# Performance work log

Measured on AMD Instinct MI355X. Metric: run time of the kernel, lower is better.

The kernel has to match this reference:

```python
import jax, jax.numpy as jnp
import numpy as np

B, CIN, H, W = 256, 1280, 7, 7
A, NCLS, HID, NGT = 9, 20, 128, 40
OUT_DIM = 5 * A + NCLS  # 65


def setup_inputs() -> dict:
    key = jax.random.key(0)
    ks = jax.random.split(key, 8)
    features = jax.random.normal(ks[0], (B, CIN, H, W), jnp.float32)
    # grid: (x, y) centers of each feature cell, in feature-map coordinates
    grid = jax.random.uniform(ks[1], (B, H, W, 2), jnp.float32) * 7.0
    # GT boxes (x1, y1, x2, y2, class), padded count NGT per image
    xy1 = jax.random.uniform(ks[2], (B, NGT, 2), jnp.float32) * 5.0
    wh = jax.random.uniform(ks[3], (B, NGT, 2), jnp.float32) * 2.0 + 0.5
    cls = jax.random.randint(ks[4], (B, NGT, 1), 0, NCLS).astype(jnp.float32)
    bboxes = jnp.concatenate([xy1, xy1 + wh, cls], axis=-1)
    # anchor shapes (w, h) as in SingleStageDetector.__init__
    anc = jnp.array([[1.0, 1], [2, 2], [3, 3], [4, 4], [5, 5],
                     [2, 3], [3, 2], [3, 5], [5, 3]], jnp.float32)
    W1 = jax.random.normal(ks[5], (HID, CIN), jnp.float32) * 0.02
    b1 = jnp.zeros((HID,), jnp.float32)
    W2 = jax.random.normal(ks[6], (OUT_DIM, HID), jnp.float32) * 0.02
    b2 = jnp.zeros((OUT_DIM,), jnp.float32)
    return dict(features=features, grid=grid, bboxes=bboxes, anc=anc,
                W1=W1, b1=b1, W2=W2, b2=b2)


def reference(features, grid, bboxes, anc, W1, b1, W2, b2):
    Bx = features.shape[0]
    # --- PredictionNetwork (inference mode; dropout is identity at eval) ---
    h = jnp.einsum('bchw,oc->bohw', features, W1) + b1[None, :, None, None]
    h = jax.nn.leaky_relu(h, negative_slope=0.01)
    out = jnp.einsum('bchw,oc->bohw', h, W2) + b2[None, :, None, None]
    conf_scores = jax.nn.sigmoid(out[:, 4 * A:5 * A])          # (B, A, H, W)
    offsets = out[:, :4 * A].reshape(Bx, A, 4, H, W)
    offsets = jnp.concatenate(
        [jax.nn.sigmoid(offsets[:, :, :2]) - 0.5, offsets[:, :, 2:]], axis=2)
    class_scores = out[:, 5 * A:]                               # (B, C, H, W)
    # --- GenerateAnchor: (B, A, H, W, 4) as (x_tl, y_tl, x_br, y_br) ---
    ctr = grid[:, None]                    # (B, 1, H, W, 2)
    half = anc[None, :, None, None, :] / 2  # (1, A, 1, 1, 2)
    anchors = jnp.concatenate([ctr - half, ctr + half], axis=-1)
    # --- IoU: (B, A*H*W, N) ---
    P = anchors.reshape(Bx, -1, 4)          # (B, AHW, 4)
    gt = bboxes[..., :4]                    # (B, N, 4)
    tl = jnp.maximum(P[:, :, None, :2], gt[:, None, :, :2])
    br = jnp.minimum(P[:, :, None, 2:], gt[:, None, :, 2:])
    inter = jnp.prod(jnp.clip(br - tl, 0.0), axis=-1)  # (B, AHW, N)
    # torch code zeroes intersections for proposals with any coord <= 0
    legal = (jnp.min(P, axis=-1) > 0)[..., None]
    inter = inter * legal
    p_area = ((P[:, :, 2] - P[:, :, 0]) * (P[:, :, 3] - P[:, :, 1]))[:, :, None]
    g_area = ((gt[:, :, 2] - gt[:, :, 0]) * (gt[:, :, 3] - gt[:, :, 1]))[:, None, :]
    iou_mat = inter / (g_area + p_area - inter)
    return (conf_scores, offsets, class_scores, iou_mat)
```

## Files before the change

kernel.cpp:

```cpp
#include <hip/hip_runtime.h>


#define CIN_  1280
#define HW_   49
#define HID_  128
#define OUTD_ 65
#define NGT_  40
#define NP_   441

#define CONF_OFF 0
#define OFFS_OFF 112896
#define CLS_OFF  564480
#define IOU_OFF  815360

#define WS_W1F_U32 81920u
#define WS_W2F_U32 5120u

typedef __bf16 bf16x8 __attribute__((ext_vector_type(8)));
typedef float  f32x4  __attribute__((ext_vector_type(4)));

__device__ __forceinline__ unsigned pack2bf(float lo, float hi) {
    unsigned a = __float_as_uint(lo);
    unsigned b = __float_as_uint(hi);
    a = (a + 0x7FFFu + ((a >> 16) & 1u)) >> 16;
    b = (b + 0x7FFFu + ((b >> 16) & 1u)) >> 16;
    return a | (b << 16);
}
__device__ __forceinline__ float sigmoidf_(float v) { return 1.f / (1.f + __expf(-v)); }

__device__ __forceinline__ bf16x8 ld_frag(const unsigned* p) {
    union { uint4 u; bf16x8 v; } x;
    x.u = *(const uint4*)p;
    return x.v;
}
__device__ __forceinline__ bf16x8 as_bf(uint4 u) {
    union { uint4 u; bf16x8 v; } x; x.u = u; return x.v;
}

__global__ __launch_bounds__(256) void prep_w(
    const float* __restrict__ W1, const float* __restrict__ W2,
    unsigned* __restrict__ ws)
{
    int X = blockIdx.x * 256 + threadIdx.x;
    if (X < (int)WS_W1F_U32) {
        int sub = X & 3, lane = (X >> 2) & 63, f = X >> 8;
        int mt = f & 7, K32 = f >> 3;
        int o = mt * 16 + (lane & 15);
        int c = K32 * 32 + (lane >> 4) * 8 + sub * 2;
        float2 v = *(const float2*)(W1 + o * CIN_ + c);
        ws[X] = pack2bf(v.x, v.y);
    } else {
        int Y = X - (int)WS_W1F_U32;
        int sub = Y & 3, lane = (Y >> 2) & 63, f = Y >> 8;
        int mt2 = f % 5, ks2 = f / 5;
        int o2 = mt2 * 16 + (lane & 15);
        int c = ks2 * 32 + (lane >> 4) * 8 + sub * 2;
        unsigned val = 0;
        if (o2 < OUTD_) {
            float2 v = *(const float2*)(W2 + o2 * HID_ + c);
            val = pack2bf(v.x, v.y);
        }
        ws[WS_W1F_U32 + Y] = val;
    }
}

__global__ __launch_bounds__(512, 8) void fused_main(
    const float* __restrict__ F,
    const float* __restrict__ grd,
    const float* __restrict__ bbox,
    const float* __restrict__ anc,
    const unsigned* __restrict__ wsW,
    const float* __restrict__ B1,
    const float* __restrict__ B2,
    float* __restrict__ out)
{
    __shared__ __align__(16) unsigned lds[16 * 640];
    unsigned* smHT = lds;

    const int tid  = threadIdx.x;
    const int b    = blockIdx.x >> 2;
    const int qtr  = blockIdx.x & 3;
    const int lane = tid & 63;
    const int w    = tid >> 6;
    const int quad = lane >> 4;
    const int m16  = lane & 15;
    const int hw0  = qtr * 16;

    const float* Fb = F + b * (CIN_ * HW_);

    #pragma unroll
    for (int g = 0; g < 4; ++g) {
        float f0[5], f1[5];
        #pragma unroll
        for (int u = 0; u < 5; ++u) {
            int i   = (g * 5 + u) * 512 + tid;
            int cp  = i >> 4;
            int row = i & 15;
            int hw  = hw0 + row;
            bool ok = hw < HW_;
            f0[u] = ok ? Fb[(2 * cp) * HW_ + hw] : 0.f;
            f1[u] = ok ? Fb[(2 * cp + 1) * HW_ + hw] : 0.f;
        }
        #pragma unroll
        for (int u = 0; u < 5; ++u) {
            int i   = (g * 5 + u) * 512 + tid;
            int cp  = i >> 4;
            int row = i & 15;
            int cb = cp >> 2, sub = cp & 3;
            lds[row * 640 + ((cb ^ (row & 7)) << 2) + sub] = pack2bf(f0[u], f1[u]);
        }
    }
    __syncthreads();

    const uint4* Ap = (const uint4*)wsW + w * 64 + lane;
    const unsigned* r0b = lds + m16 * 640;
    const int swz = (m16 & 7);

    f32x4 acc0 = (f32x4)(0.f);
    uint4 a0 = Ap[0];
    uint4 a1 = Ap[512];
    for (int k = 0; k < 40; ++k) {
        uint4 an;
        if (k < 38) an = Ap[(k + 2) * 512];
        int off = ((k * 4 + quad) ^ swz) << 2;
        acc0 = __builtin_amdgcn_mfma_f32_16x16x32_bf16(as_bf(a0), ld_frag(r0b + off), acc0, 0, 0, 0);
        a0 = a1; a1 = an;
    }

    uint4 a20 = {}, a21 = {}, a22 = {}, a23 = {};
    if (w < 5) {
        const uint4* A2p = (const uint4*)(wsW + WS_W1F_U32) + w * 64 + lane;
        a20 = A2p[0]; a21 = A2p[320]; a22 = A2p[640]; a23 = A2p[960];
    }

    __syncthreads();

    #pragma unroll
    for (int rp = 0; rp < 2; ++rp) {
        int o0 = w * 16 + quad * 4 + 2 * rp;
        float v0 = acc0[2 * rp]     + B1[o0];
        float v1 = acc0[2 * rp + 1] + B1[o0 + 1];
        v0 = v0 > 0.f ? v0 : 0.01f * v0;
        v1 = v1 > 0.f ? v1 : 0.01f * v1;
        smHT[m16 * 68 + (o0 >> 1)] = pack2bf(v0, v1);
    }
    __syncthreads();

    if (w < 5) {
        f32x4 c2 = (f32x4)(0.f);
        const unsigned* Bb = smHT + m16 * 68 + quad * 4;
        c2 = __builtin_amdgcn_mfma_f32_16x16x32_bf16(as_bf(a20), ld_frag(Bb +  0), c2, 0, 0, 0);
        c2 = __builtin_amdgcn_mfma_f32_16x16x32_bf16(as_bf(a21), ld_frag(Bb + 16), c2, 0, 0, 0);
        c2 = __builtin_amdgcn_mfma_f32_16x16x32_bf16(as_bf(a22), ld_frag(Bb + 32), c2, 0, 0, 0);
        c2 = __builtin_amdgcn_mfma_f32_16x16x32_bf16(as_bf(a23), ld_frag(Bb + 48), c2, 0, 0, 0);
        int hw = hw0 + m16;
        if (hw < HW_) {
            #pragma unroll
            for (int r = 0; r < 4; ++r) {
                int o2 = w * 16 + quad * 4 + r;
                if (o2 >= OUTD_) continue;
                float aa = c2[r] + B2[o2];
                unsigned dst; float val;
                if (o2 < 36) {
                    int an9 = o2 >> 2, kk = o2 & 3;
                    val = (kk < 2) ? (sigmoidf_(aa) - 0.5f) : aa;
                    dst = OFFS_OFF + b * 1764 + an9 * 196 + kk * 49 + hw;
                } else if (o2 < 45) {
                    val = sigmoidf_(aa);
                    dst = CONF_OFF + b * 441 + (o2 - 36) * 49 + hw;
                } else {
                    val = aa;
                    dst = CLS_OFF + b * 980 + (o2 - 45) * 49 + hw;
                }
                out[dst] = val;
            }
        }
    }

    {
        int gl = (lane < NGT_) ? lane : 0;
        const float* gb = bbox + b * 200 + gl * 5;
        float gx1 = gb[0], gy1 = gb[1], gx2 = gb[2], gy2 = gb[3];
        float gA = (gx2 - gx1) * (gy2 - gy1);
        const int pstart = (qtr * NP_) >> 2;
        const int pend   = ((qtr + 1) * NP_) >> 2;
        #pragma unroll 4
        for (int p = pstart + w; p < pend; p += 8) {
            int a9 = p / 49, r = p - a9 * 49;
            float2 ct = *(const float2*)(grd + b * 98 + 2 * r);
            float hx = anc[2 * a9] * 0.5f,  hy = anc[2 * a9 + 1] * 0.5f;
            float px1 = ct.x - hx, py1 = ct.y - hy, px2 = ct.x + hx, py2 = ct.y + hy;
            float pA = (px2 - px1) * (py2 - py1);
            float legal = (fminf(fminf(px1, py1), fminf(px2, py2)) > 0.f) ? 1.f : 0.f;
            float tlx = fmaxf(px1, gx1), tly = fmaxf(py1, gy1);
            float brx = fminf(px2, gx2), bry = fminf(py2, gy2);
            float dx = fmaxf(brx - tlx, 0.f), dy = fmaxf(bry - tly, 0.f);
            float inter = dx * dy * legal;
            float iou = inter / (gA + pA - inter);
            if (lane < NGT_)
                out[IOU_OFF + b * (NP_ * NGT_) + p * 40 + lane] = iou;
        }
    }
}

extern "C" void kernel_launch(void* const* d_in, const int* in_sizes, int n_in,
                              void* d_out, int out_size, void* d_ws, size_t ws_size,
                              hipStream_t stream) {
    const float* F  = (const float*)d_in[0];
    const float* G  = (const float*)d_in[1];
    const float* BB = (const float*)d_in[2];
    const float* AN = (const float*)d_in[3];
    const float* W1 = (const float*)d_in[4];
    const float* B1 = (const float*)d_in[5];
    const float* W2 = (const float*)d_in[6];
    const float* B2 = (const float*)d_in[7];
    float* out = (float*)d_out;
    unsigned* wsu = (unsigned*)d_ws;

    prep_w<<<340, 256, 0, stream>>>(W1, W2, wsu);
    fused_main<<<1024, 512, 0, stream>>>(F, G, BB, AN, wsu, B1, B2, out);
}
```

Before: 145.6 us.

## Process one image per block with double-buffered async feature staging into LDS

Instead of four blocks per image each gathering a strided 16-pixel slice, each block now handles a whole image. It streams contiguous 256-channel fp32 feature chunks into LDS with global_load_lds, double-buffered across five chunks. Features are converted to bf16 fragments when read from LDS, and each wave computes a 2x2 tile of MFMA outputs, so W1 fragments are fetched once per image instead of four times. The goal is to replace uncoalesced strided global reads and repeated weight traffic with coalesced async copies that overlap compute. The cost is only 256 blocks of 8 waves with about 100KB of LDS each, and padded rows that read neighbouring channel data which is then discarded. Smaller tweaks switch bf16 packing to a native conversion and IoU division to __fdividef.

```diff
diff --git a/kernel.cpp b/kernel.cpp
--- a/kernel.cpp
+++ b/kernel.cpp
@@ -16,15 +16,15 @@
 #define WS_W1F_U32 81920u
 #define WS_W2F_U32 5120u
 
+#define CHUNK_DW 12544
+
 typedef __bf16 bf16x8 __attribute__((ext_vector_type(8)));
 typedef float  f32x4  __attribute__((ext_vector_type(4)));
 
 __device__ __forceinline__ unsigned pack2bf(float lo, float hi) {
-    unsigned a = __float_as_uint(lo);
-    unsigned b = __float_as_uint(hi);
-    a = (a + 0x7FFFu + ((a >> 16) & 1u)) >> 16;
-    b = (b + 0x7FFFu + ((b >> 16) & 1u)) >> 16;
-    return a | (b << 16);
+    unsigned short a = __builtin_bit_cast(unsigned short, (__bf16)lo);
+    unsigned short b = __builtin_bit_cast(unsigned short, (__bf16)hi);
+    return (unsigned)a | ((unsigned)b << 16);
 }
 __device__ __forceinline__ float sigmoidf_(float v) { return 1.f / (1.f + __expf(-v)); }
 
@@ -35,6 +35,18 @@
 }
 __device__ __forceinline__ bf16x8 as_bf(uint4 u) {
     union { uint4 u; bf16x8 v; } x; x.u = u; return x.v;
+}
+__device__ __forceinline__ bf16x8 frag_from_f32(const float* p) {
+    union { unsigned u[4]; bf16x8 v; } x;
+    #pragma unroll
+    for (int j = 0; j < 4; ++j)
+        x.u[j] = pack2bf(p[(2 * j) * 49], p[(2 * j + 1) * 49]);
+    return x.v;
+}
+__device__ __forceinline__ void gload_lds16(const float* g, unsigned* l) {
+    __builtin_amdgcn_global_load_lds(
+        (const __attribute__((address_space(1))) unsigned*)g,
+        (__attribute__((address_space(3))) unsigned*)l, 16, 0, 0);
 }
 
 __global__ __launch_bounds__(256) void prep_w(
@@ -64,7 +76,7 @@
     }
 }
 
-__global__ __launch_bounds__(512, 8) void fused_main(
+__global__ __launch_bounds__(512, 2) void fused_main(
     const float* __restrict__ F,
     const float* __restrict__ grd,
     const float* __restrict__ bbox,
@@ -74,90 +86,102 @@
     const float* __restrict__ B2,
     float* __restrict__ out)
 {
-    __shared__ __align__(16) unsigned lds[16 * 640];
+    __shared__ __align__(16) unsigned lds[2 * CHUNK_DW + 64];
     unsigned* smHT = lds;
 
     const int tid  = threadIdx.x;
-    const int b    = blockIdx.x >> 2;
-    const int qtr  = blockIdx.x & 3;
+    const int b    = blockIdx.x;
     const int lane = tid & 63;
     const int w    = tid >> 6;
+    const int wo   = w >> 1;
+    const int wh   = w & 1;
     const int quad = lane >> 4;
     const int m16  = lane & 15;
-    const int hw0  = qtr * 16;
 
     const float* Fb = F + b * (CIN_ * HW_);
 
+    #define STAGE(c)                                                         \
+        {                                                                    \
+            const float* srcb = Fb + (c) * CHUNK_DW;                         \
+            unsigned*    dstb = lds + (((c) & 1) ? CHUNK_DW : 0);            \
+            _Pragma("unroll")                                                \
+            for (int i = 0; i < 6; ++i) {                                    \
+                int s0 = w * 1536 + i * 256;                                 \
+                gload_lds16(srcb + s0 + lane * 4, dstb + s0);                \
+            }                                                                \
+            if (w == 7) gload_lds16(srcb + 12288 + lane * 4, dstb + 12288);  \
+        }
+
+    STAGE(0);
+    __syncthreads();
+
+    const uint4* Af = (const uint4*)wsW;
+    f32x4 acc[2][2] = {{(f32x4)(0.f), (f32x4)(0.f)}, {(f32x4)(0.f), (f32x4)(0.f)}};
+
     #pragma unroll
-    for (int g = 0; g < 4; ++g) {
-        float f0[5], f1[5];
+    for (int c = 0; c < 5; ++c) {
+        uint4 Ar[8][2];
         #pragma unroll
-        for (int u = 0; u < 5; ++u) {
-            int i   = (g * 5 + u) * 512 + tid;
-            int cp  = i >> 4;
-            int row = i & 15;
-            int hw  = hw0 + row;
-            bool ok = hw < HW_;
-            f0[u] = ok ? Fb[(2 * cp) * HW_ + hw] : 0.f;
-            f1[u] = ok ? Fb[(2 * cp + 1) * HW_ + hw] : 0.f;
-        }
+        for (int kk = 0; kk < 8; ++kk) {
+            #pragma unroll
+            for (int mo = 0; mo < 2; ++mo)
+                Ar[kk][mo] = Af[(((c * 8 + kk) * 8) + (wo * 2 + mo)) * 64 + lane];
+        }
+        __builtin_amdgcn_sched_barrier(0);
+        if (c < 4) STAGE(c + 1);
+        __builtin_amdgcn_sched_barrier(0);
+
+        const float* fb = (const float*)(lds + ((c & 1) ? CHUNK_DW : 0));
         #pragma unroll
-        for (int u = 0; u < 5; ++u) {
-            int i   = (g * 5 + u) * 512 + tid;
-            int cp  = i >> 4;
-            int row = i & 15;
-            int cb = cp >> 2, sub = cp & 3;
-            lds[row * 640 + ((cb ^ (row & 7)) << 2) + sub] = pack2bf(f0[u], f1[u]);
+        for (int kk = 0; kk < 8; ++kk) {
+            bf16x8 A0 = as_bf(Ar[kk][0]);
+            bf16x8 A1 = as_bf(Ar[kk][1]);
+            #pragma unroll
+            for (int nh = 0; nh < 2; ++nh) {
+                const float* pb = fb + (kk * 32 + quad * 8) * 49
+                                     + (wh * 32 + nh * 16 + m16);
+                bf16x8 Bf = frag_from_f32(pb);
+                acc[0][nh] = __builtin_amdgcn_mfma_f32_16x16x32_bf16(A0, Bf, acc[0][nh], 0, 0, 0);
+                acc[1][nh] = __builtin_amdgcn_mfma_f32_16x16x32_bf16(A1, Bf, acc[1][nh], 0, 0, 0);
+            }
+        }
+        __builtin_amdgcn_sched_barrier(0);
+        __syncthreads();
+    }
+
+    #pragma unroll
+    for (int mo = 0; mo < 2; ++mo) {
+        #pragma unroll
+        for (int nh = 0; nh < 2; ++nh) {
+            int row = (wh * 2 + nh) * 16 + m16;
+            #pragma unroll
+            for (int rp = 0; rp < 2; ++rp) {
+                int o0 = (wo * 2 + mo) * 16 + quad * 4 + 2 * rp;
+                float v0 = acc[mo][nh][2 * rp]     + B1[o0];
+                float v1 = acc[mo][nh][2 * rp + 1] + B1[o0 + 1];
+                v0 = v0 > 0.f ? v0 : 0.01f * v0;
+                v1 = v1 > 0.f ? v1 : 0.01f * v1;
+                smHT[row * 68 + (o0 >> 1)] = pack2bf(v0, v1);
+            }
         }
     }
     __syncthreads();
 
-    const uint4* Ap = (const uint4*)wsW + w * 64 + lane;
-    const unsigned* r0b = lds + m16 * 640;
-    const int swz = (m16 & 7);
-
-    f32x4 acc0 = (f32x4)(0.f);
-    uint4 a0 = Ap[0];
-    uint4 a1 = Ap[512];
-    for (int k = 0; k < 40; ++k) {
-        uint4 an;
-        if (k < 38) an = Ap[(k + 2) * 512];
-        int off = ((k * 4 + quad) ^ swz) << 2;
-        acc0 = __builtin_amdgcn_mfma_f32_16x16x32_bf16(as_bf(a0), ld_frag(r0b + off), acc0, 0, 0, 0);
-        a0 = a1; a1 = an;
-    }
-
-    uint4 a20 = {}, a21 = {}, a22 = {}, a23 = {};
-    if (w < 5) {
-        const uint4* A2p = (const uint4*)(wsW + WS_W1F_U32) + w * 64 + lane;
-        a20 = A2p[0]; a21 = A2p[320]; a22 = A2p[640]; a23 = A2p[960];
-    }
-
-    __syncthreads();
-
-    #pragma unroll
-    for (int rp = 0; rp < 2; ++rp) {
-        int o0 = w * 16 + quad * 4 + 2 * rp;
-        float v0 = acc0[2 * rp]     + B1[o0];
-        float v1 = acc0[2 * rp + 1] + B1[o0 + 1];
-        v0 = v0 > 0.f ? v0 : 0.01f * v0;
-        v1 = v1 > 0.f ? v1 : 0.01f * v1;
-        smHT[m16 * 68 + (o0 >> 1)] = pack2bf(v0, v1);
-    }
-    __syncthreads();
-
-    if (w < 5) {
+    for (int T = w; T < 20; T += 8) {
+        int m2 = T % 5, nt2 = T / 5;
+        const uint4* A2p = (const uint4*)(wsW + WS_W1F_U32) + m2 * 64 + lane;
+        uint4 a20 = A2p[0], a21 = A2p[320], a22 = A2p[640], a23 = A2p[960];
         f32x4 c2 = (f32x4)(0.f);
-        const unsigned* Bb = smHT + m16 * 68 + quad * 4;
+        const unsigned* Bb = smHT + (nt2 * 16 + m16) * 68 + quad * 4;
         c2 = __builtin_amdgcn_mfma_f32_16x16x32_bf16(as_bf(a20), ld_frag(Bb +  0), c2, 0, 0, 0);
         c2 = __builtin_amdgcn_mfma_f32_16x16x32_bf16(as_bf(a21), ld_frag(Bb + 16), c2, 0, 0, 0);
         c2 = __builtin_amdgcn_mfma_f32_16x16x32_bf16(as_bf(a22), ld_frag(Bb + 32), c2, 0, 0, 0);
         c2 = __builtin_amdgcn_mfma_f32_16x16x32_bf16(as_bf(a23), ld_frag(Bb + 48), c2, 0, 0, 0);
-        int hw = hw0 + m16;
+        int hw = nt2 * 16 + m16;
         if (hw < HW_) {
             #pragma unroll
             for (int r = 0; r < 4; ++r) {
-                int o2 = w * 16 + quad * 4 + r;
+                int o2 = m2 * 16 + quad * 4 + r;
                 if (o2 >= OUTD_) continue;
                 float aa = c2[r] + B2[o2];
                 unsigned dst; float val;
@@ -182,10 +206,8 @@
         const float* gb = bbox + b * 200 + gl * 5;
         float gx1 = gb[0], gy1 = gb[1], gx2 = gb[2], gy2 = gb[3];
         float gA = (gx2 - gx1) * (gy2 - gy1);
-        const int pstart = (qtr * NP_) >> 2;
-        const int pend   = ((qtr + 1) * NP_) >> 2;
         #pragma unroll 4
-        for (int p = pstart + w; p < pend; p += 8) {
+        for (int p = w; p < NP_; p += 8) {
             int a9 = p / 49, r = p - a9 * 49;
             float2 ct = *(const float2*)(grd + b * 98 + 2 * r);
             float hx = anc[2 * a9] * 0.5f,  hy = anc[2 * a9 + 1] * 0.5f;
@@ -196,7 +218,7 @@
             float brx = fminf(px2, gx2), bry = fminf(py2, gy2);
             float dx = fmaxf(brx - tlx, 0.f), dy = fmaxf(bry - tly, 0.f);
             float inter = dx * dy * legal;
-            float iou = inter / (gA + pA - inter);
+            float iou = __fdividef(inter, gA + pA - inter);
             if (lane < NGT_)
                 out[IOU_OFF + b * (NP_ * NGT_) + p * 40 + lane] = iou;
         }
@@ -218,5 +240,5 @@
     unsigned* wsu = (unsigned*)d_ws;
 
     prep_w<<<340, 256, 0, stream>>>(W1, W2, wsu);
-    fused_main<<<1024, 512, 0, stream>>>(F, G, BB, AN, wsu, B1, B2, out);
-}
+    fused_main<<<256, 512, 0, stream>>>(F, G, BB, AN, wsu, B1, B2, out);
+}
```

Result: faster. 132.4 us (-9.1%).
